# Performance work log

Hardware: AMD Instinct MI355X
Metric: run time of the kernel (lower is better)

Reference implementation:

```python
import jax, jax.numpy as jnp
import numpy as np

N = 16384          # nodes
E = 262144         # edges (avg degree 16)
MUL0, MUL1 = 16, 8 # multiplicities of 0e and 1o irreps
DIM = MUL0 + 3 * MUL1  # 40
NB, RH = 10, 16    # radial basis size, radial hidden
MAX_RADIUS = 1.3
W00_N = MUL0 * MUL0
W11_N = MUL1 * MUL0
W01_N = MUL0 * MUL1
W10_N = MUL1 * MUL1
WNUM = W00_N + W11_N + W01_N + W10_N  # 576
INV_SQRT3 = 1.0 / np.sqrt(3.0)        # wigner-3j (1,1,0) / (1,0,1) factor
A_PATH = 1.0 / np.sqrt(MUL0 + MUL1)   # path/fan normalization


def split_irreps(x):
    sc = x[..., :MUL0]
    vec = x[..., MUL0:].reshape(x.shape[:-1] + (MUL1, 3))
    return sc, vec


def radial_net(emb, w1, w2):
    h = jax.nn.silu(emb @ w1 / np.sqrt(NB))
    return h @ w2 / np.sqrt(RH)  # [E, WNUM]


def fc_tp(f_sc, f_vec, sh_sc, sh_vec, w):
    # fully-connected tensor product (input irreps x SH -> output irreps), per-edge weights
    w00 = w[:, :W00_N].reshape(-1, MUL0, MUL0)
    w11 = w[:, W00_N:W00_N + W11_N].reshape(-1, MUL1, MUL0)
    w01 = w[:, W00_N + W11_N:W00_N + W11_N + W01_N].reshape(-1, MUL0, MUL1)
    w10 = w[:, -W10_N:].reshape(-1, MUL1, MUL1)
    out_sc = A_PATH * (jnp.einsum('ei,e,eio->eo', f_sc, sh_sc, w00)
                       + INV_SQRT3 * jnp.einsum('eic,ec,eio->eo', f_vec, sh_vec, w11))
    out_vec = A_PATH * (jnp.einsum('ei,ec,eio->eoc', f_sc, sh_vec, w01)
                        + jnp.einsum('eic,e,eio->eoc', f_vec, sh_sc, w10))
    return out_sc, out_vec


def dot_tp(q_sc, q_vec, k_sc, k_vec, Wd00, Wd11):
    # FullyConnectedTensorProduct(query, key, '0e') with shared weights -> scalar per edge
    s0 = jnp.einsum('ei,ej,ij->e', q_sc, k_sc, Wd00) / MUL0
    s1 = jnp.einsum('eic,ejc,ij->e', q_vec, k_vec, Wd11) / (MUL1 * np.sqrt(3.0))
    return (s0 + s1) / np.sqrt(2.0)


def soft_unit_step(x):
    xs = jnp.where(x > 0, x, 1.0)
    return jnp.where(x > 0, jnp.exp(-1.0 / xs), 0.0)


def setup_inputs():
    key = jax.random.key(0)
    ks = jax.random.split(key, 13)
    return {
        'f': jax.random.normal(ks[0], (N, DIM), jnp.float32),
        'edge_index': jax.random.randint(ks[1], (2, E), 0, N),
        'edge_length': jax.random.uniform(ks[2], (E,), jnp.float32),
        'edge_sh': jax.random.normal(ks[3], (E, 4), jnp.float32),
        'edge_length_embedded': jax.random.uniform(ks[4], (E, NB), jnp.float32),
        'Wq0': jax.random.normal(ks[5], (MUL0, MUL0), jnp.float32),
        'Wq1': jax.random.normal(ks[6], (MUL1, MUL1), jnp.float32),
        'fck_w1': jax.random.normal(ks[7], (NB, RH), jnp.float32),
        'fck_w2': jax.random.normal(ks[8], (RH, WNUM), jnp.float32),
        'fcv_w1': jax.random.normal(ks[9], (NB, RH), jnp.float32),
        'fcv_w2': jax.random.normal(ks[10], (RH, WNUM), jnp.float32),
        'Wd00': jax.random.normal(ks[11], (MUL0, MUL0), jnp.float32),
        'Wd11': jax.random.normal(ks[12], (MUL1, MUL1), jnp.float32),
    }


def reference(f, edge_index, edge_length, edge_sh, edge_length_embedded,
              Wq0, Wq1, fck_w1, fck_w2, fcv_w1, fcv_w2, Wd00, Wd11):
    f_sc, f_vec = split_irreps(f)
    # h_q: equivariant linear (per-irrep channel mixing)
    q_sc = f_sc @ Wq0 / np.sqrt(MUL0)
    q_vec = jnp.einsum('nic,io->noc', f_vec, Wq1) / np.sqrt(MUL1)
    src, dst = edge_index[0], edge_index[1]
    sh_sc, sh_vec = edge_sh[:, 0], edge_sh[:, 1:4]
    # radial MLPs -> per-edge TP weights
    wk = radial_net(edge_length_embedded, fck_w1, fck_w2)
    wv = radial_net(edge_length_embedded, fcv_w1, fcv_w2)
    k_sc, k_vec = fc_tp(f_sc[dst], f_vec[dst], sh_sc, sh_vec, wk)
    v_sc, v_vec = fc_tp(f_sc[src], f_vec[src], sh_sc, sh_vec, wv)
    cut = soft_unit_step(10.0 * (1.0 - edge_length / MAX_RADIUS))
    s = dot_tp(q_sc[dst], q_vec[dst], k_sc, k_vec, Wd00, Wd11)
    exp_ijk = cut * jnp.exp(s)                                   # [E]
    z = jax.ops.segment_sum(exp_ijk, dst, num_segments=N)        # [N]
    z = jnp.where(z == 0, 1.0, z)
    alpha = exp_ijk / z[dst]
    w_edge = jnp.sqrt(jnp.maximum(alpha, 0.0))[:, None]          # sqrt(relu(alpha))
    v_flat = jnp.concatenate([v_sc, v_vec.reshape(-1, MUL1 * 3)], axis=-1)
    f_out = jax.ops.segment_sum(w_edge * v_flat, dst, num_segments=N)
    return f_out
```

## Files before the change

kernel.cpp:

```cpp
#include <hip/hip_runtime.h>
#include <hip/hip_bf16.h>
#include <math.h>

namespace {
constexpr int NN  = 16384;
constexpr int NE  = 262144;
constexpr int DIM = 40;

constexpr float INV_SQRT3   = 0.5773502691896258f;
constexpr float A_PATH      = 0.2041241452319315f;
constexpr float INV_SQRT_NB = 0.31622776601683794f;
constexpr float H_SCALE     = 0.25f;
constexpr float QSC_S       = 0.25f;
constexpr float QV_S        = 0.35355339059327373f;
constexpr float D00_S       = 1.0f / (16.0f * 1.4142135623730951f);
constexpr float D11_S       = 1.0f / (8.0f * 1.7320508075688772f * 1.4142135623730951f);

constexpr int BKP = 392;
constexpr int K0P = 328;
constexpr int KCP = 264;
constexpr int BKTOT = 16 * K0P + 16 * KCP;
constexpr int FEP = 40;

constexpr int PREP_NODE_BLKS = NN / 256;
constexpr int PREP_BV_BLKS   = 32 * BKP / 256;
constexpr int PREP_BK_BLKS   = BKTOT / 256;
}

typedef __attribute__((ext_vector_type(8))) _Float16 f16x8;
typedef __attribute__((ext_vector_type(4))) float f32x4;

static __device__ __forceinline__ void gload_lds16(const void* g, void* l) {
  __builtin_amdgcn_global_load_lds(
      (const __attribute__((address_space(1))) unsigned*)g,
      (__attribute__((address_space(3))) unsigned*)l, 16, 0, 0);
}

__global__ __launch_bounds__(256) void prep_kernel(
    const float* __restrict__ f,
    const float* __restrict__ Wq0, const float* __restrict__ Wq1,
    const float* __restrict__ Wd00, const float* __restrict__ Wd11,
    const float* __restrict__ w2v,
    const float* __restrict__ w2k,
    float* __restrict__ qd,
    unsigned short* __restrict__ Btv,
    unsigned short* __restrict__ Btk,
    int* __restrict__ cnt)
{
  const int blk = blockIdx.x;
  if (blk < PREP_NODE_BLKS) {
    const int n = blk * 256 + threadIdx.x;
    cnt[n] = 0;

    float fs[16], fv[8][3];
    {
      const float4* fn4 = reinterpret_cast<const float4*>(f + (size_t)n * DIM);
#pragma unroll
      for (int i = 0; i < 10; i++) {
        float4 t = fn4[i];
        int base = i * 4;
#pragma unroll
        for (int k = 0; k < 4; k++) {
          float v = (k == 0) ? t.x : (k == 1) ? t.y : (k == 2) ? t.z : t.w;
          int idx = base + k;
          if (idx < 16) fs[idx] = v;
          else { int r = idx - 16; fv[r / 3][r % 3] = v; }
        }
      }
    }

    float out[40];
    {
      float qsc[16];
#pragma unroll
      for (int o = 0; o < 16; o++) {
        float a = 0.f;
#pragma unroll
        for (int i = 0; i < 16; i++) a += fs[i] * Wq0[i * 16 + o];
        qsc[o] = a * QSC_S;
      }
#pragma unroll
      for (int j = 0; j < 16; j++) {
        float a = 0.f;
#pragma unroll
        for (int i = 0; i < 16; i++) a += qsc[i] * Wd00[i * 16 + j];
        out[j] = a * D00_S;
      }
    }
    {
      float qv[8][3];
#pragma unroll
      for (int o = 0; o < 8; o++)
#pragma unroll
        for (int c = 0; c < 3; c++) {
          float a = 0.f;
#pragma unroll
          for (int i = 0; i < 8; i++) a += fv[i][c] * Wq1[i * 8 + o];
          qv[o][c] = a * QV_S;
        }
#pragma unroll
      for (int j = 0; j < 8; j++)
#pragma unroll
        for (int c = 0; c < 3; c++) {
          float a = 0.f;
#pragma unroll
          for (int i = 0; i < 8; i++) a += qv[i][c] * Wd11[i * 8 + j];
          out[16 + j * 3 + c] = a * D11_S;
        }
    }

    float4* op = reinterpret_cast<float4*>(qd + (size_t)n * DIM);
#pragma unroll
    for (int i = 0; i < 10; i++)
      op[i] = make_float4(out[4 * i], out[4 * i + 1], out[4 * i + 2], out[4 * i + 3]);

  } else if (blk < PREP_NODE_BLKS + PREP_BV_BLKS) {
    int t = (blk - PREP_NODE_BLKS) * 256 + threadIdx.x;
    int col = t / BKP, kp = t % BKP;
    float val = 0.f;
    if (kp < 384 && col < 24) {
      if (kp < 256) {
        int r = kp >> 4, i = kp & 15;
        if (col < 16) val = A_PATH * w2v[r * 576 + i * 16 + col];
        else          val = A_PATH * w2v[r * 576 + 384 + i * 8 + (col - 16)];
      } else {
        int k2 = kp - 256; int r = k2 >> 3, i = k2 & 7;
        if (col < 16) val = A_PATH * INV_SQRT3 * w2v[r * 576 + 256 + i * 16 + col];
        else          val = A_PATH * w2v[r * 576 + 512 + i * 8 + (col - 16)];
      }
    }
    _Float16 hv = (_Float16)val;
    Btv[t] = __builtin_bit_cast(unsigned short, hv);

  } else {
    int t = (blk - PREP_NODE_BLKS - PREP_BV_BLKS) * 256 + threadIdx.x;
    float val = 0.f;
    if (t < 16 * K0P) {
      int r = t / K0P, k = t % K0P;
      if (k < 256)      { int i = k >> 4, o = k & 15; val = w2k[r * 576 + i * 16 + o]; }
      else if (k < 320) { int kk = k - 256; int i = kk >> 3, o = kk & 7;
                          val = w2k[r * 576 + 512 + i * 8 + o]; }
    } else {
      int t2 = t - 16 * K0P;
      int r = t2 / KCP, k = t2 % KCP;
      if (k < 128)      { int i = k >> 4, o = k & 15;
                          val = INV_SQRT3 * w2k[r * 576 + 256 + i * 16 + o]; }
      else if (k < 256) { int kk = k - 128; int i = kk >> 3, o = kk & 7;
                          val = w2k[r * 576 + 384 + i * 8 + o]; }
    }
    _Float16 hv = (_Float16)val;
    Btk[t] = __builtin_bit_cast(unsigned short, hv);
  }
}

__global__ __launch_bounds__(256) void qq_mfma_kernel(
    const float* __restrict__ f,
    const float* __restrict__ qd,
    const unsigned short* __restrict__ Btk,
    float* __restrict__ qq)
{
  __shared__ __attribute__((aligned(16))) unsigned short BL[BKTOT];
  __shared__ float fsT[16][65];
  __shared__ float fvT[24][65];
  __shared__ float qd0T[16][65];
  __shared__ float qdvT[24][65];

  const int tid  = threadIdx.x;
  const int base = blockIdx.x * 64;

  {
    const char* src = (const char*)Btk;
    char* dst = (char*)BL;
#pragma unroll
    for (int k2 = 0; k2 < 4; k2++) {
      int off = (k2 * 256 + tid) * 16;
      gload_lds16(src + off, dst + off);
    }
    if (tid < 160) {
      int off = (1024 + tid) * 16;
      gload_lds16(src + off, dst + off);
    }
  }

  const int m = tid & 63;
  const int q = tid >> 6;
  const int n = base + m;

  if (q == 0) {
    const float4* f4 = reinterpret_cast<const float4*>(f + (size_t)n * DIM);
    float v[40];
#pragma unroll
    for (int i = 0; i < 10; i++) {
      float4 t = f4[i];
      v[4 * i] = t.x; v[4 * i + 1] = t.y; v[4 * i + 2] = t.z; v[4 * i + 3] = t.w;
    }
#pragma unroll
    for (int i = 0; i < 16; i++) fsT[i][m] = v[i];
#pragma unroll
    for (int k = 0; k < 24; k++) fvT[(k % 3) * 8 + (k / 3)][m] = v[16 + k];
  } else if (q == 1) {
    const float4* q4 = reinterpret_cast<const float4*>(qd + (size_t)n * DIM);
    float v[40];
#pragma unroll
    for (int i = 0; i < 10; i++) {
      float4 t = q4[i];
      v[4 * i] = t.x; v[4 * i + 1] = t.y; v[4 * i + 2] = t.z; v[4 * i + 3] = t.w;
    }
#pragma unroll
    for (int i = 0; i < 16; i++) qd0T[i][m] = v[i];
#pragma unroll
    for (int k = 0; k < 24; k++) qdvT[(k % 3) * 8 + (k / 3)][m] = v[16 + k];
  }
  __syncthreads();

  const int w    = tid >> 6;
  const int l    = tid & 63;
  const int row  = l & 15;
  const int kb   = l >> 4;
  const int mrow = w * 16 + row;
  const int col  = l & 15;

  f32x4 p0  = {0.f, 0.f, 0.f, 0.f};
  f32x4 pcA = {0.f, 0.f, 0.f, 0.f}, pcB = {0.f, 0.f, 0.f, 0.f}, pcC = {0.f, 0.f, 0.f, 0.f};

#pragma unroll
  for (int s = 0; s < 10; s++) {
    f16x8 a;
    if (s < 8) {
      const int i  = 2 * s + (kb >> 1);
      const int o0 = (kb & 1) * 8;
      const float fsv = fsT[i][mrow];
#pragma unroll
      for (int j = 0; j < 8; j++) a[j] = (_Float16)(fsv * qd0T[o0 + j][mrow]);
    } else {
      const int i = (s - 8) * 4 + kb;
      const float fv0 = fvT[i][mrow], fv1 = fvT[8 + i][mrow], fv2 = fvT[16 + i][mrow];
#pragma unroll
      for (int j = 0; j < 8; j++)
        a[j] = (_Float16)(fv0 * qdvT[j][mrow] + fv1 * qdvT[8 + j][mrow]
                          + fv2 * qdvT[16 + j][mrow]);
    }
    const int k0 = s * 32 + kb * 8;
    f16x8 b = *reinterpret_cast<const f16x8*>(&BL[col * K0P + k0]);
    p0 = __builtin_amdgcn_mfma_f32_16x16x32_f16(a, b, p0, 0, 0, 0);
  }

#pragma unroll
  for (int c = 0; c < 3; c++) {
    f32x4* pc = (c == 0) ? &pcA : (c == 1) ? &pcB : &pcC;
#pragma unroll
    for (int s = 0; s < 8; s++) {
      f16x8 a;
      if (s < 4) {
        const int i  = 2 * s + (kb >> 1);
        const int o0 = (kb & 1) * 8;
        const float fvv = fvT[c * 8 + i][mrow];
#pragma unroll
        for (int j = 0; j < 8; j++) a[j] = (_Float16)(fvv * qd0T[o0 + j][mrow]);
      } else {
        const int i = (s - 4) * 4 + kb;
        const float fsv = fsT[i][mrow];
#pragma unroll
        for (int j = 0; j < 8; j++) a[j] = (_Float16)(fsv * qdvT[c * 8 + j][mrow]);
      }
      const int k0 = s * 32 + kb * 8;
      f16x8 b = *reinterpret_cast<const f16x8*>(&BL[16 * K0P + col * KCP + k0]);
      *pc = __builtin_amdgcn_mfma_f32_16x16x32_f16(a, b, *pc, 0, 0, 0);
    }
  }

#pragma unroll
  for (int j = 0; j < 4; j++) {
    const int me = w * 16 + kb * 4 + j;
    float4 outv = make_float4(A_PATH * p0[j], A_PATH * pcA[j],
                              A_PATH * pcB[j], A_PATH * pcC[j]);
    reinterpret_cast<float4*>(qq)[(size_t)(base + me) * 16 + col] = outv;
  }
}

__global__ __launch_bounds__(256) void hist_kernel(const int* __restrict__ ei,
                                                   int* __restrict__ cnt,
                                                   float* __restrict__ out)
{
  const int e = blockIdx.x * 256 + threadIdx.x;
#pragma unroll
  for (int i = 0; i < 3; i++) {
    int idx = e + i * NE;
    if (idx < NN * DIM) out[idx] = 0.f;
  }
  atomicAdd(&cnt[ei[NE + e]], 1);
}

__global__ __launch_bounds__(1024) void scan_kernel(const int* __restrict__ cnt,
                                                    int* __restrict__ off,
                                                    float* __restrict__ z)
{
  __shared__ int part[1024];
  const int t = threadIdx.x;
  const int base = t * 16;
  int loc[16];
  int s = 0;
#pragma unroll
  for (int k = 0; k < 16; k++) { loc[k] = s; s += cnt[base + k]; }
  part[t] = s;
  __syncthreads();
  for (int d = 1; d < 1024; d <<= 1) {
    int v = (t >= d) ? part[t - d] : 0;
    __syncthreads();
    part[t] += v;
    __syncthreads();
  }
  int excl = (t == 0) ? 0 : part[t - 1];
#pragma unroll
  for (int k = 0; k < 16; k++) {
    off[base + k] = excl + loc[k];
    z[base + k] = 0.f;
  }
}

__global__ __launch_bounds__(256) void edge_kernel(
    const int*   __restrict__ ei,
    const float* __restrict__ elen,
    const float* __restrict__ esh,
    const float* __restrict__ emb,
    const float* __restrict__ w1k,
    const float* __restrict__ w1v,
    const float* __restrict__ qq,
    int*   __restrict__ off,
    float4* __restrict__ edata,
    float* __restrict__ z)
{
  const int gid = blockIdx.x * 256 + threadIdx.x;

  const int src = ei[gid];
  const int dst = ei[NE + gid];
  const int rk = atomicAdd(&off[dst], 1);

  float el[10];
  const float2* e2 = reinterpret_cast<const float2*>(emb + (size_t)gid * 10);
#pragma unroll
  for (int b = 0; b < 5; b++) { float2 t = e2[b]; el[2 * b] = t.x; el[2 * b + 1] = t.y; }

  float h[16];
#pragma unroll
  for (int j = 0; j < 16; j++) {
    float a = 0.f;
#pragma unroll
    for (int b = 0; b < 10; b++) a += el[b] * w1k[b * 16 + j];
    a *= INV_SQRT_NB;
    float sig = 1.0f / (1.0f + __expf(-a));
    h[j] = a * sig * H_SCALE;
  }

  float4 sh4 = reinterpret_cast<const float4*>(esh)[gid];
  const float4* q4 = reinterpret_cast<const float4*>(qq + (size_t)dst * 64);
  float s = 0.f;
#pragma unroll
  for (int r = 0; r < 16; r++) {
    float4 qv = q4[r];
    s += h[r] * (sh4.x * qv.x + sh4.y * qv.y + sh4.z * qv.z + sh4.w * qv.w);
  }

  float len = elen[gid];
  float x = 10.0f * (1.0f - len * (1.0f / 1.3f));
  float cut = (x > 0.f) ? __expf(-1.0f / x) : 0.f;
  float ev = cut * __expf(s);
  atomicAdd(&z[dst], ev);

  f16x8 hv0, hv1;
#pragma unroll
  for (int j = 0; j < 16; j++) {
    float a = 0.f;
#pragma unroll
    for (int b = 0; b < 10; b++) a += el[b] * w1v[b * 16 + j];
    a *= INV_SQRT_NB;
    float sig = 1.0f / (1.0f + __expf(-a));
    _Float16 hh = (_Float16)(a * sig * H_SCALE);
    if (j < 8) hv0[j] = hh; else hv1[j - 8] = hh;
  }

  float4* ep = edata + (size_t)rk * 4;
  ep[0] = __builtin_bit_cast(float4, hv0);
  ep[1] = __builtin_bit_cast(float4, hv1);
  ep[2] = sh4;
  ep[3] = make_float4(__int_as_float(src), __int_as_float(dst), ev, 0.f);
}

__global__ __launch_bounds__(512) void v_mfma_kernel(
    const float* __restrict__ f,
    const float4* __restrict__ edata,
    const float* __restrict__ z,
    const unsigned short* __restrict__ Bt,
    float* __restrict__ fout)
{
  __shared__ __attribute__((aligned(16))) unsigned short BtL[32][BKP];
  __shared__ __attribute__((aligned(16))) _Float16 h_s[2][64][18];
  __shared__ __attribute__((aligned(16))) _Float16 feE[2][64][FEP];
  __shared__ float scal[2][64][5];
  __shared__ int   nid[2][64];
  __shared__ float rows[2][64][41];
  __shared__ int seg_start[2][64], seg_len[2][64], seg_nid[2][64];
  __shared__ int nseg_s[2];

  const int tid = threadIdx.x;

  {
    const char* src = (const char*)Bt;
    char* dst = (char*)&BtL[0][0];
#pragma unroll
    for (int k = 0; k < 3; k++) {
      int off = (k * 512 + tid) * 16;
      gload_lds16(src + off, dst + off);
    }
    if (tid < 32) {
      int off = (1536 + tid) * 16;
      gload_lds16(src + off, dst + off);
    }
  }

  const int hf  = tid >> 8;
  const int t2  = tid & 255;
  const int m   = t2 & 63;
  const int q   = t2 >> 6;
  const int base = blockIdx.x * 128 + hf * 64;
  const float4* ed = edata + (size_t)(base + m) * 4;

  if (q == 0) {
    float4 v3 = ed[3];
    float4 sh4 = ed[2];
    int dn = __float_as_int(v3.y);
    float zz = z[dn]; zz = (zz == 0.f) ? 1.f : zz;
    float ev = v3.z;
    float wgt = sqrtf(fmaxf(ev / zz, 0.f));
    scal[hf][m][0] = sh4.x; scal[hf][m][1] = sh4.y;
    scal[hf][m][2] = sh4.z; scal[hf][m][3] = sh4.w;
    scal[hf][m][4] = wgt;
    nid[hf][m] = dn;
  } else if (q == 3) {
    int sn = __float_as_int(ed[3].x);
    const float4* f4 = reinterpret_cast<const float4*>(f + (size_t)sn * DIM);
    float v[40];
#pragma unroll
    for (int i = 0; i < 10; i++) {
      float4 t = f4[i];
      v[4 * i] = t.x; v[4 * i + 1] = t.y; v[4 * i + 2] = t.z; v[4 * i + 3] = t.w;
    }
#pragma unroll
    for (int i = 0; i < 16; i++) feE[hf][m][i] = (_Float16)v[i];
#pragma unroll
    for (int k = 0; k < 24; k++)
      feE[hf][m][16 + (k % 3) * 8 + (k / 3)] = (_Float16)v[16 + k];
  } else if (q == 1) {
    f16x8 h0 = __builtin_bit_cast(f16x8, ed[0]);
    f16x8 h1 = __builtin_bit_cast(f16x8, ed[1]);
#pragma unroll
    for (int j = 0; j < 8; j++) {
      h_s[hf][m][j]     = h0[j];
      h_s[hf][m][8 + j] = h1[j];
    }
  }
  __syncthreads();

  const int w    = t2 >> 6;
  const int l    = t2 & 63;
  const int row  = l & 15;
  const int kb   = l >> 4;
  const int mrow = w * 16 + row;
  const int col  = l & 15;

  const int i0 = (kb & 1) * 8;
  f16x8 afs = *reinterpret_cast<const f16x8*>(&feE[hf][mrow][i0]);
  f16x8 afv0 = *reinterpret_cast<const f16x8*>(&feE[hf][mrow][16]);
  f16x8 afv1 = *reinterpret_cast<const f16x8*>(&feE[hf][mrow][24]);
  f16x8 afv2 = *reinterpret_cast<const f16x8*>(&feE[hf][mrow][32]);

  f32x4 pfs0 = {0.f, 0.f, 0.f, 0.f}, pfs1 = {0.f, 0.f, 0.f, 0.f};
  f32x4 pc0_0 = {0.f, 0.f, 0.f, 0.f}, pc0_1 = {0.f, 0.f, 0.f, 0.f}, pc0_2 = {0.f, 0.f, 0.f, 0.f};
  f32x4 pc1_0 = {0.f, 0.f, 0.f, 0.f}, pc1_1 = {0.f, 0.f, 0.f, 0.f}, pc1_2 = {0.f, 0.f, 0.f, 0.f};

#pragma unroll
  for (int s = 0; s < 8; s++) {
    const int r  = 2 * s + (kb >> 1);
    const _Float16 hr = h_s[hf][mrow][r];
    f16x8 a;
#pragma unroll
    for (int j = 0; j < 8; j++) a[j] = hr * afs[j];
    const int k0 = s * 32 + kb * 8;
    f16x8 b0 = *reinterpret_cast<const f16x8*>(&BtL[col][k0]);
    f16x8 b1 = *reinterpret_cast<const f16x8*>(&BtL[16 + col][k0]);
    pfs0 = __builtin_amdgcn_mfma_f32_16x16x32_f16(a, b0, pfs0, 0, 0, 0);
    pfs1 = __builtin_amdgcn_mfma_f32_16x16x32_f16(a, b1, pfs1, 0, 0, 0);
  }

#pragma unroll
  for (int s = 0; s < 4; s++) {
    const int r = 4 * s + kb;
    const _Float16 hr = h_s[hf][mrow][r];
    const int k0 = 256 + s * 32 + kb * 8;
    f16x8 b0 = *reinterpret_cast<const f16x8*>(&BtL[col][k0]);
    f16x8 b1 = *reinterpret_cast<const f16x8*>(&BtL[16 + col][k0]);
#pragma unroll
    for (int c = 0; c < 3; c++) {
      const f16x8 av = (c == 0) ? afv0 : (c == 1) ? afv1 : afv2;
      f16x8 a;
#pragma unroll
      for (int j = 0; j < 8; j++) a[j] = hr * av[j];
      f32x4* p0 = (c == 0) ? &pc0_0 : (c == 1) ? &pc0_1 : &pc0_2;
      f32x4* p1 = (c == 0) ? &pc1_0 : (c == 1) ? &pc1_1 : &pc1_2;
      *p0 = __builtin_amdgcn_mfma_f32_16x16x32_f16(a, b0, *p0, 0, 0, 0);
      *p1 = __builtin_amdgcn_mfma_f32_16x16x32_f16(a, b1, *p1, 0, 0, 0);
    }
  }

#pragma unroll
  for (int j = 0; j < 4; j++) {
    const int me = w * 16 + kb * 4 + j;
    const float sh0 = scal[hf][me][0], sh1 = scal[hf][me][1];
    const float sh2 = scal[hf][me][2], sh3 = scal[hf][me][3];
    const float wg = scal[hf][me][4];
    float vsc = sh0 * pfs0[j] + sh1 * pc0_0[j] + sh2 * pc0_1[j] + sh3 * pc0_2[j];
    rows[hf][me][col] = wg * vsc;
    if (col < 8) {
      rows[hf][me][16 + col * 3 + 0] = wg * (sh1 * pfs1[j] + sh0 * pc1_0[j]);
      rows[hf][me][16 + col * 3 + 1] = wg * (sh2 * pfs1[j] + sh0 * pc1_1[j]);
      rows[hf][me][16 + col * 3 + 2] = wg * (sh3 * pfs1[j] + sh0 * pc1_2[j]);
    }
  }
  __syncthreads();

  if (t2 < 64) {
    bool head = (m == 0) || (nid[hf][m] != nid[hf][m - 1]);
    unsigned long long mask = __ballot(head);
    if (t2 == 0) nseg_s[hf] = __popcll(mask);
    if (head) {
      int idx = __popcll(mask & ((1ull << m) - 1ull));
      unsigned long long higher = (m == 63) ? 0ull : (mask >> (m + 1));
      int len = higher ? __ffsll((long long)higher) : (64 - m);
      seg_start[hf][idx] = m; seg_len[hf][idx] = len; seg_nid[hf][idx] = nid[hf][m];
    }
  }
  __syncthreads();

  const int nseg = nseg_s[hf];
  const int d = t2 & 63;
  const int g = t2 >> 6;
  if (d < DIM) {
    for (int s = g; s < nseg; s += 4) {
      const int st = seg_start[hf][s], ln = seg_len[hf][s];
      float acc = 0.f;
      for (int k2 = 0; k2 < ln; k2++) acc += rows[hf][st + k2][d];
      float* fo = &fout[(size_t)seg_nid[hf][s] * DIM + d];
      if (s > 0 && s < nseg - 1) *fo = acc;
      else atomicAdd(fo, acc);
    }
  }
}

extern "C" void kernel_launch(void* const* d_in, const int* in_sizes, int n_in,
                              void* d_out, int out_size, void* d_ws, size_t ws_size,
                              hipStream_t stream) {
  const float* f      = (const float*)d_in[0];
  const int*   ei     = (const int*)d_in[1];
  const float* elen   = (const float*)d_in[2];
  const float* esh    = (const float*)d_in[3];
  const float* emb    = (const float*)d_in[4];
  const float* Wq0    = (const float*)d_in[5];
  const float* Wq1    = (const float*)d_in[6];
  const float* fck_w1 = (const float*)d_in[7];
  const float* fck_w2 = (const float*)d_in[8];
  const float* fcv_w1 = (const float*)d_in[9];
  const float* fcv_w2 = (const float*)d_in[10];
  const float* Wd00   = (const float*)d_in[11];
  const float* Wd11   = (const float*)d_in[12];

  float* out = (float*)d_out;

  char* ws = (char*)d_ws;
  float* qq       = (float*)ws;  ws += (size_t)NN * 64 * 4;
  float* qd       = (float*)ws;  ws += (size_t)NN * DIM * 4;
  float* z        = (float*)ws;  ws += (size_t)NN * 4;
  int*   cnt      = (int*)ws;    ws += (size_t)NN * 4;
  int*   off      = (int*)ws;    ws += (size_t)NN * 4;
  ws = (char*)(((size_t)ws + 63) & ~(size_t)63);
  float4* edata   = (float4*)ws; ws += (size_t)NE * 64;
  unsigned short* Btv = (unsigned short*)ws;  ws += (size_t)32 * BKP * 2;
  unsigned short* Btk = (unsigned short*)ws;  ws += (size_t)BKTOT * 2;

  prep_kernel<<<PREP_NODE_BLKS + PREP_BV_BLKS + PREP_BK_BLKS, 256, 0, stream>>>(
      f, Wq0, Wq1, Wd00, Wd11, fcv_w2, fck_w2, qd, Btv, Btk, cnt);
  hist_kernel<<<NE / 256, 256, 0, stream>>>(ei, cnt, out);
  scan_kernel<<<1, 1024, 0, stream>>>(cnt, off, z);
  qq_mfma_kernel<<<NN / 64, 256, 0, stream>>>(f, qd, Btk, qq);
  edge_kernel<<<NE / 256, 256, 0, stream>>>(ei, elen, esh, emb, fck_w1, fcv_w1,
                                            qq, off, edata, z);
  v_mfma_kernel<<<NE / 128, 512, 0, stream>>>(f, edata, z, Btv, out);
}
```

Measured before the change: 100.3 us.

## Merge histogram into qq kernel, store qq and node features in fp16

Merges the histogram/zeroing kernel into the qq MFMA kernel as extra blocks, removing one launch and letting both run concurrently. The qq table is stored in fp16 instead of fp32, halving the per-edge gather in edge_kernel. The node features are pre-converted and permuted to fp16 in prep, so the v_mfma kernel gathers 80 bytes per edge with vector copies instead of 160 bytes plus conversion. The cost is reduced precision in qq, plus an extra fp16 feature buffer written in prep.

```diff
diff --git a/kernel.cpp b/kernel.cpp
--- a/kernel.cpp
+++ b/kernel.cpp
@@ -21,13 +21,17 @@
 constexpr int KCP = 264;
 constexpr int BKTOT = 16 * K0P + 16 * KCP;
 constexpr int FEP = 40;
+constexpr int FHP = 48;
 
 constexpr int PREP_NODE_BLKS = NN / 256;
 constexpr int PREP_BV_BLKS   = 32 * BKP / 256;
 constexpr int PREP_BK_BLKS   = BKTOT / 256;
+
+constexpr int HIST_BLKS = NE / 256;
 }
 
 typedef __attribute__((ext_vector_type(8))) _Float16 f16x8;
+typedef __attribute__((ext_vector_type(4))) _Float16 f16x4;
 typedef __attribute__((ext_vector_type(4))) float f32x4;
 
 static __device__ __forceinline__ void gload_lds16(const void* g, void* l) {
@@ -43,6 +47,7 @@
     const float* __restrict__ w2v,
     const float* __restrict__ w2k,
     float* __restrict__ qd,
+    _Float16* __restrict__ fhalf,
     unsigned short* __restrict__ Btv,
     unsigned short* __restrict__ Btk,
     int* __restrict__ cnt)
@@ -67,6 +72,22 @@
           else { int r = idx - 16; fv[r / 3][r % 3] = v; }
         }
       }
+    }
+
+    {
+      _Float16 fh[FHP];
+#pragma unroll
+      for (int i = 0; i < 16; i++) fh[i] = (_Float16)fs[i];
+#pragma unroll
+      for (int i = 0; i < 8; i++)
+#pragma unroll
+        for (int c = 0; c < 3; c++) fh[16 + c * 8 + i] = (_Float16)fv[i][c];
+#pragma unroll
+      for (int i = 40; i < FHP; i++) fh[i] = (_Float16)0.f;
+      f16x8* fp = reinterpret_cast<f16x8*>(fhalf + (size_t)n * FHP);
+#pragma unroll
+      for (int i = 0; i < FHP / 8; i++)
+        fp[i] = *reinterpret_cast<const f16x8*>(&fh[i * 8]);
     }
 
     float out[40];
@@ -153,11 +174,14 @@
   }
 }
 
-__global__ __launch_bounds__(256) void qq_mfma_kernel(
+__global__ __launch_bounds__(256) void qq_hist_kernel(
+    const int*   __restrict__ ei,
+    int*         __restrict__ cnt,
+    float*       __restrict__ out,
     const float* __restrict__ f,
     const float* __restrict__ qd,
     const unsigned short* __restrict__ Btk,
-    float* __restrict__ qq)
+    _Float16*    __restrict__ qq16)
 {
   __shared__ __attribute__((aligned(16))) unsigned short BL[BKTOT];
   __shared__ float fsT[16][65];
@@ -165,8 +189,19 @@
   __shared__ float qd0T[16][65];
   __shared__ float qdvT[24][65];
 
+  if (blockIdx.x < HIST_BLKS) {
+    const int e = blockIdx.x * 256 + threadIdx.x;
+#pragma unroll
+    for (int i = 0; i < 3; i++) {
+      int idx = e + i * NE;
+      if (idx < NN * DIM) out[idx] = 0.f;
+    }
+    atomicAdd(&cnt[ei[NE + e]], 1);
+    return;
+  }
+
   const int tid  = threadIdx.x;
-  const int base = blockIdx.x * 64;
+  const int base = (blockIdx.x - HIST_BLKS) * 64;
 
   {
     const char* src = (const char*)Btk;
@@ -272,23 +307,13 @@
 #pragma unroll
   for (int j = 0; j < 4; j++) {
     const int me = w * 16 + kb * 4 + j;
-    float4 outv = make_float4(A_PATH * p0[j], A_PATH * pcA[j],
-                              A_PATH * pcB[j], A_PATH * pcC[j]);
-    reinterpret_cast<float4*>(qq)[(size_t)(base + me) * 16 + col] = outv;
-  }
-}
-
-__global__ __launch_bounds__(256) void hist_kernel(const int* __restrict__ ei,
-                                                   int* __restrict__ cnt,
-                                                   float* __restrict__ out)
-{
-  const int e = blockIdx.x * 256 + threadIdx.x;
-#pragma unroll
-  for (int i = 0; i < 3; i++) {
-    int idx = e + i * NE;
-    if (idx < NN * DIM) out[idx] = 0.f;
-  }
-  atomicAdd(&cnt[ei[NE + e]], 1);
+    f16x4 o;
+    o[0] = (_Float16)(A_PATH * p0[j]);
+    o[1] = (_Float16)(A_PATH * pcA[j]);
+    o[2] = (_Float16)(A_PATH * pcB[j]);
+    o[3] = (_Float16)(A_PATH * pcC[j]);
+    *reinterpret_cast<f16x4*>(qq16 + ((size_t)(base + me) * 16 + col) * 4) = o;
+  }
 }
 
 __global__ __launch_bounds__(1024) void scan_kernel(const int* __restrict__ cnt,
@@ -325,7 +350,7 @@
     const float* __restrict__ emb,
     const float* __restrict__ w1k,
     const float* __restrict__ w1v,
-    const float* __restrict__ qq,
+    const _Float16* __restrict__ qq16,
     int*   __restrict__ off,
     float4* __restrict__ edata,
     float* __restrict__ z)
@@ -353,12 +378,15 @@
   }
 
   float4 sh4 = reinterpret_cast<const float4*>(esh)[gid];
-  const float4* q4 = reinterpret_cast<const float4*>(qq + (size_t)dst * 64);
+  const f16x8* q8 = reinterpret_cast<const f16x8*>(qq16 + (size_t)dst * 64);
   float s = 0.f;
 #pragma unroll
-  for (int r = 0; r < 16; r++) {
-    float4 qv = q4[r];
-    s += h[r] * (sh4.x * qv.x + sh4.y * qv.y + sh4.z * qv.z + sh4.w * qv.w);
+  for (int i = 0; i < 8; i++) {
+    f16x8 qv = q8[i];
+    s += h[2 * i] * (sh4.x * (float)qv[0] + sh4.y * (float)qv[1]
+                   + sh4.z * (float)qv[2] + sh4.w * (float)qv[3]);
+    s += h[2 * i + 1] * (sh4.x * (float)qv[4] + sh4.y * (float)qv[5]
+                       + sh4.z * (float)qv[6] + sh4.w * (float)qv[7]);
   }
 
   float len = elen[gid];
@@ -387,7 +415,7 @@
 }
 
 __global__ __launch_bounds__(512) void v_mfma_kernel(
-    const float* __restrict__ f,
+    const _Float16* __restrict__ fhalf,
     const float4* __restrict__ edata,
     const float* __restrict__ z,
     const unsigned short* __restrict__ Bt,
@@ -438,18 +466,10 @@
     nid[hf][m] = dn;
   } else if (q == 3) {
     int sn = __float_as_int(ed[3].x);
-    const float4* f4 = reinterpret_cast<const float4*>(f + (size_t)sn * DIM);
-    float v[40];
-#pragma unroll
-    for (int i = 0; i < 10; i++) {
-      float4 t = f4[i];
-      v[4 * i] = t.x; v[4 * i + 1] = t.y; v[4 * i + 2] = t.z; v[4 * i + 3] = t.w;
-    }
-#pragma unroll
-    for (int i = 0; i < 16; i++) feE[hf][m][i] = (_Float16)v[i];
-#pragma unroll
-    for (int k = 0; k < 24; k++)
-      feE[hf][m][16 + (k % 3) * 8 + (k / 3)] = (_Float16)v[16 + k];
+    const f16x8* fp8 = reinterpret_cast<const f16x8*>(fhalf + (size_t)sn * FHP);
+    f16x8* fe = reinterpret_cast<f16x8*>(&feE[hf][m][0]);
+#pragma unroll
+    for (int i = 0; i < 5; i++) fe[i] = fp8[i];
   } else if (q == 1) {
     f16x8 h0 = __builtin_bit_cast(f16x8, ed[0]);
     f16x8 h1 = __builtin_bit_cast(f16x8, ed[1]);
@@ -576,22 +596,23 @@
   float* out = (float*)d_out;
 
   char* ws = (char*)d_ws;
-  float* qq       = (float*)ws;  ws += (size_t)NN * 64 * 4;
   float* qd       = (float*)ws;  ws += (size_t)NN * DIM * 4;
   float* z        = (float*)ws;  ws += (size_t)NN * 4;
   int*   cnt      = (int*)ws;    ws += (size_t)NN * 4;
   int*   off      = (int*)ws;    ws += (size_t)NN * 4;
   ws = (char*)(((size_t)ws + 63) & ~(size_t)63);
   float4* edata   = (float4*)ws; ws += (size_t)NE * 64;
+  _Float16* qq16  = (_Float16*)ws; ws += (size_t)NN * 64 * 2;
+  _Float16* fhalf = (_Float16*)ws; ws += (size_t)NN * FHP * 2;
   unsigned short* Btv = (unsigned short*)ws;  ws += (size_t)32 * BKP * 2;
   unsigned short* Btk = (unsigned short*)ws;  ws += (size_t)BKTOT * 2;
 
   prep_kernel<<<PREP_NODE_BLKS + PREP_BV_BLKS + PREP_BK_BLKS, 256, 0, stream>>>(
-      f, Wq0, Wq1, Wd00, Wd11, fcv_w2, fck_w2, qd, Btv, Btk, cnt);
-  hist_kernel<<<NE / 256, 256, 0, stream>>>(ei, cnt, out);
+      f, Wq0, Wq1, Wd00, Wd11, fcv_w2, fck_w2, qd, fhalf, Btv, Btk, cnt);
+  qq_hist_kernel<<<HIST_BLKS + NN / 64, 256, 0, stream>>>(
+      ei, cnt, out, f, qd, Btk, qq16);
   scan_kernel<<<1, 1024, 0, stream>>>(cnt, off, z);
-  qq_mfma_kernel<<<NN / 64, 256, 0, stream>>>(f, qd, Btk, qq);
   edge_kernel<<<NE / 256, 256, 0, stream>>>(ei, elen, esh, emb, fck_w1, fcv_w1,
-                                            qq, off, edata, z);
-  v_mfma_kernel<<<NE / 128, 512, 0, stream>>>(f, edata, z, Btv, out);
-}
+                                            qq16, off, edata, z);
+  v_mfma_kernel<<<NE / 128, 512, 0, stream>>>(fhalf, edata, z, Btv, out);
+}
```

Result: no change. 101.1 us, median of 2 (+0.7%).
